# Optimization experiments

Measured on AMD Instinct MI355X. Metric: run time of the kernel, lower is better.

## Reference

```python
import jax, jax.numpy as jnp
import numpy as np

B, S, H, V = 256, 15, 512, 50257

def setup_inputs() -> dict:
    key = jax.random.key(0)
    ks = jax.random.split(key, 12)
    sc_h = 1.0 / np.sqrt(H)
    sc_in = 1.0 / np.sqrt(2 * H)
    return {
        "input_tokens": jax.random.randint(ks[0], (B, 1), 0, V),
        "hidden": jax.random.normal(ks[1], (1, B, H), jnp.float32),
        "encoder_outputs": jax.random.normal(ks[2], (B, S, H), jnp.float32),
        "emb_table": jax.random.normal(ks[3], (V, H), jnp.float32),
        "attn_W": jax.random.uniform(ks[4], (H, H), jnp.float32, -sc_h, sc_h),
        "attn_b": jax.random.uniform(ks[5], (H,), jnp.float32, -sc_h, sc_h),
        "W_ih": jax.random.uniform(ks[6], (3 * H, 2 * H), jnp.float32, -sc_in, sc_in),
        "W_hh": jax.random.uniform(ks[7], (3 * H, H), jnp.float32, -sc_h, sc_h),
        "b_ih": jax.random.uniform(ks[8], (3 * H,), jnp.float32, -sc_h, sc_h),
        "b_hh": jax.random.uniform(ks[9], (3 * H,), jnp.float32, -sc_h, sc_h),
        "out_W": jax.random.uniform(ks[10], (V, H), jnp.float32, -sc_h, sc_h),
        "out_b": jax.random.uniform(ks[11], (V,), jnp.float32, -sc_h, sc_h),
    }


def reference(input_tokens, hidden, encoder_outputs, emb_table, attn_W, attn_b,
              W_ih, W_hh, b_ih, b_hh, out_W, out_b):
    # Embedding (dropout is identity in eval/reference mode): [B,1,H]
    embedded = emb_table[input_tokens]
    h = hidden[0]  # [B,H]

    # Bahdanau-style scores, vectorized over the seq dim instead of the python loop:
    # energies[b,s] = attn(enc[b,s]);  score[b,s] = <h[b], energies[b,s]>
    energies = jnp.einsum("bsh,oh->bso", encoder_outputs, attn_W) + attn_b  # [B,S,H]
    attn_scores = jnp.einsum("bso,bo->bs", energies, h)                      # [B,S]
    attn_weights = jax.nn.softmax(attn_scores, axis=1)                       # [B,S]

    # context = weights @ encoder_outputs: [B,1,H]
    context = jnp.einsum("bs,bsh->bh", attn_weights, encoder_outputs)[:, None, :]

    # GRU single step (PyTorch gate order: r, z, n)
    x = jnp.concatenate([embedded, context], axis=2)[:, 0]  # [B,2H]
    gi = x @ W_ih.T + b_ih   # [B,3H]
    gh = h @ W_hh.T + b_hh   # [B,3H]
    i_r, i_z, i_n = jnp.split(gi, 3, axis=1)
    h_r, h_z, h_n = jnp.split(gh, 3, axis=1)
    r = jax.nn.sigmoid(i_r + h_r)
    z = jax.nn.sigmoid(i_z + h_z)
    n = jnp.tanh(i_n + r * h_n)
    h_new = (1.0 - z) * n + z * h            # [B,H]

    logits = h_new[:, None, :] @ out_W.T + out_b   # [B,1,V]
    log_probs = jax.nn.log_softmax(logits, axis=-1)
    return log_probs, h_new[None], attn_weights
```

## Files before the change

kernel.cpp:

```cpp
#include <hip/hip_runtime.h>

#define V_SIZE 50257
#define B_SIZE 256
#define S_LEN  15
#define H_DIM  512
#define NBLK_LG 786

typedef __attribute__((ext_vector_type(8))) short bf16x8;
typedef __attribute__((ext_vector_type(4))) float f32x4;

__device__ __forceinline__ unsigned short f2bf(float f) {
    unsigned int u = __float_as_uint(f);
    u += 0x7fffu + ((u >> 16) & 1u);
    return (unsigned short)(u >> 16);
}

__global__ __launch_bounds__(256) void u_kernel(
    const float* __restrict__ hidden, const float* __restrict__ attn_W,
    float* __restrict__ u)
{
    __shared__ float h_s[16][H_DIM];
    const int tid = threadIdx.x;
    const int b0 = blockIdx.y * 16, n0 = blockIdx.x * 32;
    const float4* hv = (const float4*)(hidden + (size_t)b0 * H_DIM);
    float4* hs4 = (float4*)&h_s[0][0];
    #pragma unroll
    for (int i = 0; i < 8; ++i) hs4[tid + i * 256] = hv[tid + i * 256];
    __syncthreads();
    const int n = n0 + (tid & 31);
    const int m = (tid >> 5) * 2;
    float a0 = 0.f, a1 = 0.f;
    #pragma unroll 8
    for (int o = 0; o < H_DIM; ++o) {
        float w = attn_W[(size_t)o * H_DIM + n];
        a0 += h_s[m][o] * w;
        a1 += h_s[m + 1][o] * w;
    }
    u[(size_t)(b0 + m) * H_DIM + n] = a0;
    u[(size_t)(b0 + m + 1) * H_DIM + n] = a1;
}

__global__ __launch_bounds__(256) void attn_kernel(
    const float* __restrict__ hidden, const float* __restrict__ enc,
    const float* __restrict__ u, const int* __restrict__ tokens,
    const float* __restrict__ emb, float* __restrict__ attnw_out,
    unsigned short* __restrict__ x_bf, unsigned short* __restrict__ h_bf)
{
    const int b = blockIdx.x, tid = threadIdx.x;
    __shared__ float u_s[H_DIM];
    __shared__ float sc_s[S_LEN];
    __shared__ float w_s[S_LEN];
    u_s[tid]       = u[(size_t)b * H_DIM + tid];
    u_s[tid + 256] = u[(size_t)b * H_DIM + tid + 256];
    h_bf[(size_t)b * H_DIM + tid]       = f2bf(hidden[(size_t)b * H_DIM + tid]);
    h_bf[(size_t)b * H_DIM + tid + 256] = f2bf(hidden[(size_t)b * H_DIM + tid + 256]);
    const int tok = tokens[b];
    x_bf[(size_t)b * 2 * H_DIM + tid]       = f2bf(emb[(size_t)tok * H_DIM + tid]);
    x_bf[(size_t)b * 2 * H_DIM + tid + 256] = f2bf(emb[(size_t)tok * H_DIM + tid + 256]);
    __syncthreads();
    const int wave = tid >> 6, lane = tid & 63;
    for (int s = wave; s < S_LEN; s += 4) {
        const float* e = enc + ((size_t)b * S_LEN + s) * H_DIM;
        float acc = 0.f;
        #pragma unroll
        for (int k = 0; k < H_DIM / 64; ++k) acc += e[lane + k * 64] * u_s[lane + k * 64];
        #pragma unroll
        for (int off = 32; off; off >>= 1) acc += __shfl_down(acc, off);
        if (lane == 0) sc_s[s] = acc;
    }
    __syncthreads();
    float mx = -1e30f;
    for (int s = 0; s < S_LEN; ++s) mx = fmaxf(mx, sc_s[s]);
    float sum = 0.f;
    for (int s = 0; s < S_LEN; ++s) sum += __expf(sc_s[s] - mx);
    const float inv = 1.f / sum;
    if (tid < S_LEN) {
        float w = __expf(sc_s[tid] - mx) * inv;
        w_s[tid] = w;
        attnw_out[b * S_LEN + tid] = w;
    }
    __syncthreads();
    #pragma unroll
    for (int hh = 0; hh < 2; ++hh) {
        int h = tid + hh * 256;
        float c = 0.f;
        #pragma unroll
        for (int s = 0; s < S_LEN; ++s)
            c += w_s[s] * enc[((size_t)b * S_LEN + s) * H_DIM + h];
        x_bf[(size_t)b * 2 * H_DIM + H_DIM + h] = f2bf(c);
    }
}

struct GemmP {
    const unsigned short* A; const float* B; const float* bias; float* C;
    int N; int K;
};

template<int BM, int BN, int BK, int WR, int WC>
__global__ __launch_bounds__(256) void gemm_nt(GemmP p0, GemmP p1)
{
    GemmP p = (blockIdx.z == 0) ? p0 : p1;
    constexpr int LDA = BK + 8;
    __shared__ __align__(16) unsigned short As[BM][LDA];
    __shared__ __align__(16) unsigned short Bs[BN][LDA];
    const int tid = threadIdx.x;
    const int bn0 = blockIdx.x * BN;
    const int bm0 = blockIdx.y * BM;
    const int wave = tid >> 6, lane = tid & 63;
    const int wm = (wave / WC) * (BM / WR);
    const int wn = (wave % WC) * (BN / WC);
    constexpr int MF = BM / WR / 16, NF = BN / WC / 16;
    const int n16 = lane & 15, quad = lane >> 4;

    f32x4 acc[MF][NF] = {};

    for (int k0 = 0; k0 < p.K; k0 += BK) {
        #pragma unroll
        for (int it = 0; it < BM / 32; ++it) {
            int v = it * 256 + tid;
            int row = v >> 3, seg = v & 7;
            *(uint4*)&As[row][seg * 8] =
                *(const uint4*)(p.A + (size_t)(bm0 + row) * p.K + k0 + seg * 8);
        }
        #pragma unroll
        for (int it = 0; it < BN / 32; ++it) {
            int v = it * 256 + tid;
            int row = v >> 3, seg = v & 7;
            int gv = bn0 + row;
            float4 w0 = make_float4(0, 0, 0, 0), w1 = make_float4(0, 0, 0, 0);
            if (gv < p.N) {
                const float4* src = (const float4*)(p.B + (size_t)gv * p.K + k0 + seg * 8);
                w0 = src[0]; w1 = src[1];
            }
            uint4 pk;
            pk.x = (unsigned)f2bf(w0.x) | ((unsigned)f2bf(w0.y) << 16);
            pk.y = (unsigned)f2bf(w0.z) | ((unsigned)f2bf(w0.w) << 16);
            pk.z = (unsigned)f2bf(w1.x) | ((unsigned)f2bf(w1.y) << 16);
            pk.w = (unsigned)f2bf(w1.z) | ((unsigned)f2bf(w1.w) << 16);
            *(uint4*)&Bs[row][seg * 8] = pk;
        }
        __syncthreads();
        #pragma unroll
        for (int kk = 0; kk < BK; kk += 32) {
            bf16x8 af[MF], bfr[NF];
            #pragma unroll
            for (int i = 0; i < MF; ++i)
                af[i] = *(const bf16x8*)&As[wm + i * 16 + n16][kk + quad * 8];
            #pragma unroll
            for (int j = 0; j < NF; ++j)
                bfr[j] = *(const bf16x8*)&Bs[wn + j * 16 + n16][kk + quad * 8];
            #pragma unroll
            for (int i = 0; i < MF; ++i)
                #pragma unroll
                for (int j = 0; j < NF; ++j)
                    acc[i][j] = __builtin_amdgcn_mfma_f32_16x16x32_bf16(
                        af[i], bfr[j], acc[i][j], 0, 0, 0);
        }
        __syncthreads();
    }
    #pragma unroll
    for (int i = 0; i < MF; ++i) {
        const int r0 = bm0 + wm + i * 16 + quad * 4;
        #pragma unroll
        for (int j = 0; j < NF; ++j) {
            const int c = bn0 + wn + j * 16 + n16;
            if (c < p.N) {
                const float bv = p.bias[c];
                #pragma unroll
                for (int r = 0; r < 4; ++r)
                    p.C[(size_t)(r0 + r) * p.N + c] = acc[i][j][r] + bv;
            }
        }
    }
}

template<bool PART>
__global__ __launch_bounds__(256, 4) void gemm_lg(
    const unsigned short* __restrict__ A, const float* __restrict__ B,
    const float* __restrict__ bias, float* __restrict__ C,
    float* __restrict__ pm, float* __restrict__ ps)
{
    constexpr int BN = 64, BK = 128;
    constexpr int LDB = BK + 8;
    __shared__ __align__(16) unsigned short Bs[BN][LDB];
    const int tid = threadIdx.x;
    const int bn0 = blockIdx.x * BN;
    const int wave = tid >> 6, lane = tid & 63;
    const int wm = wave * 64;
    const int n16 = lane & 15, quad = lane >> 4;

    f32x4 acc[4][4] = {};
    const unsigned short* arow[4];
    #pragma unroll
    for (int i = 0; i < 4; ++i) arow[i] = A + (size_t)(wm + i * 16 + n16) * H_DIM;

    for (int k0 = 0; k0 < H_DIM; k0 += BK) {
        #pragma unroll
        for (int it = 0; it < 4; ++it) {
            int v = it * 256 + tid;
            int row = v >> 4, seg = v & 15;
            int gv = bn0 + row;
            float4 w0 = make_float4(0, 0, 0, 0), w1 = make_float4(0, 0, 0, 0);
            if (gv < V_SIZE) {
                const float4* src = (const float4*)(B + (size_t)gv * H_DIM + k0 + seg * 8);
                w0 = src[0]; w1 = src[1];
            }
            uint4 pk;
            pk.x = (unsigned)f2bf(w0.x) | ((unsigned)f2bf(w0.y) << 16);
            pk.y = (unsigned)f2bf(w0.z) | ((unsigned)f2bf(w0.w) << 16);
            pk.z = (unsigned)f2bf(w1.x) | ((unsigned)f2bf(w1.y) << 16);
            pk.w = (unsigned)f2bf(w1.z) | ((unsigned)f2bf(w1.w) << 16);
            *(uint4*)&Bs[row][seg * 8] = pk;
        }
        __syncthreads();
        #pragma unroll
        for (int kk = 0; kk < BK; kk += 32) {
            bf16x8 af[4], bfr[4];
            #pragma unroll
            for (int i = 0; i < 4; ++i)
                af[i] = *(const bf16x8*)(arow[i] + k0 + kk + quad * 8);
            #pragma unroll
            for (int j = 0; j < 4; ++j)
                bfr[j] = *(const bf16x8*)&Bs[j * 16 + n16][kk + quad * 8];
            #pragma unroll
            for (int i = 0; i < 4; ++i)
                #pragma unroll
                for (int j = 0; j < 4; ++j)
                    acc[i][j] = __builtin_amdgcn_mfma_f32_16x16x32_bf16(
                        af[i], bfr[j], acc[i][j], 0, 0, 0);
        }
        __syncthreads();
    }

    int cj[4]; float bvv[4]; bool okj[4];
    #pragma unroll
    for (int j = 0; j < 4; ++j) {
        cj[j] = bn0 + j * 16 + n16;
        okj[j] = cj[j] < V_SIZE;
        bvv[j] = okj[j] ? bias[cj[j]] : 0.f;
    }
    #pragma unroll
    for (int i = 0; i < 4; ++i) {
        const int r0 = wm + i * 16 + quad * 4;
        if (PART) {
            #pragma unroll
            for (int r = 0; r < 4; ++r) {
                float m = -1e30f;
                #pragma unroll
                for (int j = 0; j < 4; ++j)
                    if (okj[j]) m = fmaxf(m, acc[i][j][r] + bvv[j]);
                #pragma unroll
                for (int d = 1; d < 16; d <<= 1) m = fmaxf(m, __shfl_xor(m, d));
                float s = 0.f;
                #pragma unroll
                for (int j = 0; j < 4; ++j)
                    if (okj[j]) s += __expf(acc[i][j][r] + bvv[j] - m);
                #pragma unroll
                for (int d = 1; d < 16; d <<= 1) s += __shfl_xor(s, d);
                if (n16 == 0) {
                    pm[(size_t)blockIdx.x * B_SIZE + r0 + r] = m;
                    ps[(size_t)blockIdx.x * B_SIZE + r0 + r] = s;
                }
            }
        }
        #pragma unroll
        for (int j = 0; j < 4; ++j) if (okj[j]) {
            #pragma unroll
            for (int r = 0; r < 4; ++r)
                C[(size_t)(r0 + r) * V_SIZE + cj[j]] = acc[i][j][r] + bvv[j];
        }
    }
}

__global__ __launch_bounds__(256) void gru_kernel(
    const float* __restrict__ gi, const float* __restrict__ gh,
    const float* __restrict__ hidden, float* __restrict__ hnew_out,
    unsigned short* __restrict__ hnew_bf)
{
    const int idx = blockIdx.x * 256 + threadIdx.x;
    const int b = idx >> 9, h = idx & 511;
    const float* gib = gi + (size_t)b * 3 * H_DIM;
    const float* ghb = gh + (size_t)b * 3 * H_DIM;
    float r = 1.f / (1.f + __expf(-(gib[h] + ghb[h])));
    float z = 1.f / (1.f + __expf(-(gib[H_DIM + h] + ghb[H_DIM + h])));
    float n = gib[2 * H_DIM + h] + r * ghb[2 * H_DIM + h];
    n = 1.f - 2.f / (1.f + __expf(2.f * n));
    float hp = hidden[idx];
    float hn = (1.f - z) * n + z * hp;
    hnew_out[idx] = hn;
    hnew_bf[idx] = f2bf(hn);
}

__global__ __launch_bounds__(1024) void finalize_kernel(
    float* __restrict__ logits, const float* __restrict__ pm,
    const float* __restrict__ ps)
{
    const int b = blockIdx.x, tid = threadIdx.x;
    float m = -1e30f, s = 0.f;
    for (int i = tid; i < NBLK_LG; i += 1024) {
        float mm = pm[(size_t)i * B_SIZE + b], ss = ps[(size_t)i * B_SIZE + b];
        float nm = fmaxf(m, mm);
        s = s * __expf(m - nm) + ss * __expf(mm - nm);
        m = nm;
    }
    const int lane = tid & 63, wave = tid >> 6;
    #pragma unroll
    for (int off = 32; off; off >>= 1) {
        float m2 = __shfl_down(m, off), s2 = __shfl_down(s, off);
        float nm = fmaxf(m, m2);
        s = s * __expf(m - nm) + s2 * __expf(m2 - nm);
        m = nm;
    }
    __shared__ float msh[16], ssh[16], lse_sh;
    if (lane == 0) { msh[wave] = m; ssh[wave] = s; }
    __syncthreads();
    if (tid == 0) {
        float M = msh[0], S = ssh[0];
        for (int w = 1; w < 16; ++w) {
            float nm = fmaxf(M, msh[w]);
            S = S * __expf(M - nm) + ssh[w] * __expf(msh[w] - nm);
            M = nm;
        }
        lse_sh = M + logf(S);
    }
    __syncthreads();
    const float lse = lse_sh;
    constexpr int HALF = (V_SIZE + 1) / 2;
    const int start = blockIdx.y * HALF;
    const int end = min(V_SIZE, start + HALF);
    float* row = logits + (size_t)b * V_SIZE;
    for (int c = start + tid; c < end; c += 1024) row[c] -= lse;
}

__global__ __launch_bounds__(1024) void logsoftmax_kernel(float* __restrict__ logits)
{
    const int b = blockIdx.x, tid = threadIdx.x;
    float* row = logits + (size_t)b * V_SIZE;
    float m = -1e30f, s = 0.f;
    for (int c = tid; c < V_SIZE; c += 1024) {
        float x = row[c];
        float nm = fmaxf(m, x);
        s = s * __expf(m - nm) + __expf(x - nm);
        m = nm;
    }
    const int lane = tid & 63, wave = tid >> 6;
    #pragma unroll
    for (int off = 32; off; off >>= 1) {
        float m2 = __shfl_down(m, off), s2 = __shfl_down(s, off);
        float nm = fmaxf(m, m2);
        s = s * __expf(m - nm) + s2 * __expf(m2 - nm);
        m = nm;
    }
    __shared__ float msh[16], ssh[16], lse_sh;
    if (lane == 0) { msh[wave] = m; ssh[wave] = s; }
    __syncthreads();
    if (tid == 0) {
        float M = msh[0], S = ssh[0];
        for (int w = 1; w < 16; ++w) {
            float nm = fmaxf(M, msh[w]);
            S = S * __expf(M - nm) + ssh[w] * __expf(msh[w] - nm);
            M = nm;
        }
        lse_sh = M + logf(S);
    }
    __syncthreads();
    const float lse = lse_sh;
    for (int c = tid; c < V_SIZE; c += 1024) row[c] -= lse;
}

constexpr size_t OFF_U      = 0;
constexpr size_t OFF_XBF    = 524288;
constexpr size_t OFF_HBF    = 1048576;
constexpr size_t OFF_HNEWBF = 1310720;
constexpr size_t OFF_GI     = 1572864;
constexpr size_t OFF_GH     = 3145728;
constexpr size_t OFF_PM     = 4718592;
constexpr size_t OFF_PS     = 5523456;
constexpr size_t WS_NEED    = 6328320;

extern "C" void kernel_launch(void* const* d_in, const int* in_sizes, int n_in,
                              void* d_out, int out_size, void* d_ws, size_t ws_size,
                              hipStream_t stream) {
    const int*   tokens = (const int*)d_in[0];
    const float* hidden = (const float*)d_in[1];
    const float* enc    = (const float*)d_in[2];
    const float* emb    = (const float*)d_in[3];
    const float* attn_W = (const float*)d_in[4];
    const float* W_ih   = (const float*)d_in[6];
    const float* W_hh   = (const float*)d_in[7];
    const float* b_ih   = (const float*)d_in[8];
    const float* b_hh   = (const float*)d_in[9];
    const float* out_W  = (const float*)d_in[10];
    const float* out_b  = (const float*)d_in[11];

    float* out = (float*)d_out;
    float* logp      = out;
    float* hnew_out  = out + (size_t)B_SIZE * V_SIZE;
    float* attnw_out = hnew_out + (size_t)B_SIZE * H_DIM;

    char* ws = (char*)d_ws;
    float*          u_ws    = (float*)(ws + OFF_U);
    unsigned short* x_bf    = (unsigned short*)(ws + OFF_XBF);
    unsigned short* h_bf    = (unsigned short*)(ws + OFF_HBF);
    unsigned short* hnew_bf = (unsigned short*)(ws + OFF_HNEWBF);
    float*          gi_ws   = (float*)(ws + OFF_GI);
    float*          gh_ws   = (float*)(ws + OFF_GH);
    float*          pm_ws   = (float*)(ws + OFF_PM);
    float*          ps_ws   = (float*)(ws + OFF_PS);

    u_kernel<<<dim3(16, 16), 256, 0, stream>>>(hidden, attn_W, u_ws);
    attn_kernel<<<dim3(256), 256, 0, stream>>>(hidden, enc, u_ws, tokens, emb,
                                               attnw_out, x_bf, h_bf);
    GemmP gi_p { x_bf, W_ih, b_ih, gi_ws, 3 * H_DIM, 2 * H_DIM };
    GemmP gh_p { h_bf, W_hh, b_hh, gh_ws, 3 * H_DIM, H_DIM };
    gemm_nt<64, 64, 64, 2, 2><<<dim3(24, 4, 2), 256, 0, stream>>>(gi_p, gh_p);
    gru_kernel<<<dim3(512), 256, 0, stream>>>(gi_ws, gh_ws, hidden, hnew_out, hnew_bf);

    if (ws_size >= WS_NEED) {
        gemm_lg<true><<<dim3(NBLK_LG), 256, 0, stream>>>(
            hnew_bf, out_W, out_b, logp, pm_ws, ps_ws);
        finalize_kernel<<<dim3(256, 2), 1024, 0, stream>>>(logp, pm_ws, ps_ws);
    } else {
        gemm_lg<false><<<dim3(NBLK_LG), 256, 0, stream>>>(
            hnew_bf, out_W, out_b, logp, nullptr, nullptr);
        logsoftmax_kernel<<<dim3(256), 1024, 0, stream>>>(logp);
    }
}
```

Baseline: 369.7 us.

## Fuse output GEMM and log-softmax via cooperative grid sync; stage encoder in LDS

```diff
diff --git a/kernel.cpp b/kernel.cpp
--- a/kernel.cpp
+++ b/kernel.cpp
@@ -1,4 +1,5 @@
 #include <hip/hip_runtime.h>
+#include <hip/hip_cooperative_groups.h>
 
 #define V_SIZE 50257
 #define B_SIZE 256
@@ -47,9 +48,19 @@
     unsigned short* __restrict__ x_bf, unsigned short* __restrict__ h_bf)
 {
     const int b = blockIdx.x, tid = threadIdx.x;
+    __shared__ float e_s[S_LEN][H_DIM];
     __shared__ float u_s[H_DIM];
     __shared__ float sc_s[S_LEN];
     __shared__ float w_s[S_LEN];
+    {
+        const float4* ev = (const float4*)(enc + (size_t)b * S_LEN * H_DIM);
+        float4* es4 = (float4*)&e_s[0][0];
+        #pragma unroll
+        for (int i = 0; i < 8; ++i) {
+            int idx = i * 256 + tid;
+            if (idx < S_LEN * H_DIM / 4) es4[idx] = ev[idx];
+        }
+    }
     u_s[tid]       = u[(size_t)b * H_DIM + tid];
     u_s[tid + 256] = u[(size_t)b * H_DIM + tid + 256];
     h_bf[(size_t)b * H_DIM + tid]       = f2bf(hidden[(size_t)b * H_DIM + tid]);
@@ -60,10 +71,10 @@
     __syncthreads();
     const int wave = tid >> 6, lane = tid & 63;
     for (int s = wave; s < S_LEN; s += 4) {
-        const float* e = enc + ((size_t)b * S_LEN + s) * H_DIM;
         float acc = 0.f;
         #pragma unroll
-        for (int k = 0; k < H_DIM / 64; ++k) acc += e[lane + k * 64] * u_s[lane + k * 64];
+        for (int k = 0; k < H_DIM / 64; ++k)
+            acc += e_s[s][lane + k * 64] * u_s[lane + k * 64];
         #pragma unroll
         for (int off = 32; off; off >>= 1) acc += __shfl_down(acc, off);
         if (lane == 0) sc_s[s] = acc;
@@ -86,7 +97,7 @@
         float c = 0.f;
         #pragma unroll
         for (int s = 0; s < S_LEN; ++s)
-            c += w_s[s] * enc[((size_t)b * S_LEN + s) * H_DIM + h];
+            c += w_s[s] * e_s[s][h];
         x_bf[(size_t)b * 2 * H_DIM + H_DIM + h] = f2bf(c);
     }
 }
@@ -174,6 +185,144 @@
     }
 }
 
+__global__ __launch_bounds__(256, 4) void gemm_lg_coop(
+    const unsigned short* __restrict__ A, const float* __restrict__ B,
+    const float* __restrict__ bias, float* __restrict__ C,
+    float* __restrict__ pm, float* __restrict__ ps, float* __restrict__ lse_g)
+{
+    constexpr int BN = 64, BK = 128;
+    constexpr int LDB = BK + 8;
+    __shared__ __align__(16) unsigned short Bs[BN][LDB];
+    __shared__ float red_m[4], red_s[4];
+    const int tid = threadIdx.x;
+    const int bn0 = blockIdx.x * BN;
+    const int wave = tid >> 6, lane = tid & 63;
+    const int wm = wave * 64;
+    const int n16 = lane & 15, quad = lane >> 4;
+
+    f32x4 acc[4][4] = {};
+    const unsigned short* arow[4];
+    #pragma unroll
+    for (int i = 0; i < 4; ++i) arow[i] = A + (size_t)(wm + i * 16 + n16) * H_DIM;
+
+    for (int k0 = 0; k0 < H_DIM; k0 += BK) {
+        #pragma unroll
+        for (int it = 0; it < 4; ++it) {
+            int v = it * 256 + tid;
+            int row = v >> 4, seg = v & 15;
+            int gv = bn0 + row;
+            float4 w0 = make_float4(0, 0, 0, 0), w1 = make_float4(0, 0, 0, 0);
+            if (gv < V_SIZE) {
+                const float4* src = (const float4*)(B + (size_t)gv * H_DIM + k0 + seg * 8);
+                w0 = src[0]; w1 = src[1];
+            }
+            uint4 pk;
+            pk.x = (unsigned)f2bf(w0.x) | ((unsigned)f2bf(w0.y) << 16);
+            pk.y = (unsigned)f2bf(w0.z) | ((unsigned)f2bf(w0.w) << 16);
+            pk.z = (unsigned)f2bf(w1.x) | ((unsigned)f2bf(w1.y) << 16);
+            pk.w = (unsigned)f2bf(w1.z) | ((unsigned)f2bf(w1.w) << 16);
+            *(uint4*)&Bs[row][seg * 8] = pk;
+        }
+        __syncthreads();
+        #pragma unroll
+        for (int kk = 0; kk < BK; kk += 32) {
+            bf16x8 af[4], bfr[4];
+            #pragma unroll
+            for (int i = 0; i < 4; ++i)
+                af[i] = *(const bf16x8*)(arow[i] + k0 + kk + quad * 8);
+            #pragma unroll
+            for (int j = 0; j < 4; ++j)
+                bfr[j] = *(const bf16x8*)&Bs[j * 16 + n16][kk + quad * 8];
+            #pragma unroll
+            for (int i = 0; i < 4; ++i)
+                #pragma unroll
+                for (int j = 0; j < 4; ++j)
+                    acc[i][j] = __builtin_amdgcn_mfma_f32_16x16x32_bf16(
+                        af[i], bfr[j], acc[i][j], 0, 0, 0);
+        }
+        __syncthreads();
+    }
+
+    int cj[4]; float bvv[4]; bool okj[4];
+    #pragma unroll
+    for (int j = 0; j < 4; ++j) {
+        cj[j] = bn0 + j * 16 + n16;
+        okj[j] = cj[j] < V_SIZE;
+        bvv[j] = okj[j] ? bias[cj[j]] : 0.f;
+    }
+    #pragma unroll
+    for (int i = 0; i < 4; ++i) {
+        const int r0 = wm + i * 16 + quad * 4;
+        #pragma unroll
+        for (int r = 0; r < 4; ++r) {
+            float m = -1e30f;
+            #pragma unroll
+            for (int j = 0; j < 4; ++j)
+                if (okj[j]) m = fmaxf(m, acc[i][j][r] + bvv[j]);
+            #pragma unroll
+            for (int d = 1; d < 16; d <<= 1) m = fmaxf(m, __shfl_xor(m, d));
+            float s = 0.f;
+            #pragma unroll
+            for (int j = 0; j < 4; ++j)
+                if (okj[j]) s += __expf(acc[i][j][r] + bvv[j] - m);
+            #pragma unroll
+            for (int d = 1; d < 16; d <<= 1) s += __shfl_xor(s, d);
+            if (n16 == 0) {
+                pm[(size_t)blockIdx.x * B_SIZE + r0 + r] = m;
+                ps[(size_t)blockIdx.x * B_SIZE + r0 + r] = s;
+            }
+        }
+    }
+
+    cooperative_groups::this_grid().sync();
+
+    if (blockIdx.x < B_SIZE) {
+        const int b = blockIdx.x;
+        float m = -1e30f, s = 0.f;
+        for (int i = tid; i < NBLK_LG; i += 256) {
+            float mm = pm[(size_t)i * B_SIZE + b], ss = ps[(size_t)i * B_SIZE + b];
+            float nm = fmaxf(m, mm);
+            s = s * __expf(m - nm) + ss * __expf(mm - nm);
+            m = nm;
+        }
+        #pragma unroll
+        for (int off = 32; off; off >>= 1) {
+            float m2 = __shfl_down(m, off), s2 = __shfl_down(s, off);
+            float nm = fmaxf(m, m2);
+            s = s * __expf(m - nm) + s2 * __expf(m2 - nm);
+            m = nm;
+        }
+        if (lane == 0) { red_m[wave] = m; red_s[wave] = s; }
+        __syncthreads();
+        if (tid == 0) {
+            float M = red_m[0], S = red_s[0];
+            #pragma unroll
+            for (int w = 1; w < 4; ++w) {
+                float nm = fmaxf(M, red_m[w]);
+                S = S * __expf(M - nm) + red_s[w] * __expf(red_m[w] - nm);
+                M = nm;
+            }
+            lse_g[b] = M + logf(S);
+        }
+    }
+
+    cooperative_groups::this_grid().sync();
+
+    #pragma unroll
+    for (int i = 0; i < 4; ++i) {
+        const int r0 = wm + i * 16 + quad * 4;
+        float ls[4];
+        #pragma unroll
+        for (int r = 0; r < 4; ++r) ls[r] = lse_g[r0 + r];
+        #pragma unroll
+        for (int j = 0; j < 4; ++j) if (okj[j]) {
+            #pragma unroll
+            for (int r = 0; r < 4; ++r)
+                C[(size_t)(r0 + r) * V_SIZE + cj[j]] = acc[i][j][r] + bvv[j] - ls[r];
+        }
+    }
+}
+
 template<bool PART>
 __global__ __launch_bounds__(256, 4) void gemm_lg(
     const unsigned short* __restrict__ A, const float* __restrict__ B,
@@ -325,7 +474,7 @@
     }
     __syncthreads();
     const float lse = lse_sh;
-    constexpr int HALF = (V_SIZE + 1) / 2;
+    constexpr int HALF = 25132;
     const int start = blockIdx.y * HALF;
     const int end = min(V_SIZE, start + HALF);
     float* row = logits + (size_t)b * V_SIZE;
@@ -376,7 +525,9 @@
 constexpr size_t OFF_GH     = 3145728;
 constexpr size_t OFF_PM     = 4718592;
 constexpr size_t OFF_PS     = 5523456;
-constexpr size_t WS_NEED    = 6328320;
+constexpr size_t OFF_LSE    = 6328320;
+constexpr size_t WS_NEED      = 6328320;
+constexpr size_t WS_NEED_COOP = 6329344;
 
 extern "C" void kernel_launch(void* const* d_in, const int* in_sizes, int n_in,
                               void* d_out, int out_size, void* d_ws, size_t ws_size,
@@ -407,6 +558,7 @@
     float*          gh_ws   = (float*)(ws + OFF_GH);
     float*          pm_ws   = (float*)(ws + OFF_PM);
     float*          ps_ws   = (float*)(ws + OFF_PS);
+    float*          lse_ws  = (float*)(ws + OFF_LSE);
 
     u_kernel<<<dim3(16, 16), 256, 0, stream>>>(hidden, attn_W, u_ws);
     attn_kernel<<<dim3(256), 256, 0, stream>>>(hidden, enc, u_ws, tokens, emb,
@@ -416,13 +568,28 @@
     gemm_nt<64, 64, 64, 2, 2><<<dim3(24, 4, 2), 256, 0, stream>>>(gi_p, gh_p);
     gru_kernel<<<dim3(512), 256, 0, stream>>>(gi_ws, gh_ws, hidden, hnew_out, hnew_bf);
 
-    if (ws_size >= WS_NEED) {
-        gemm_lg<true><<<dim3(NBLK_LG), 256, 0, stream>>>(
-            hnew_bf, out_W, out_b, logp, pm_ws, ps_ws);
-        finalize_kernel<<<dim3(256, 2), 1024, 0, stream>>>(logp, pm_ws, ps_ws);
-    } else {
-        gemm_lg<false><<<dim3(NBLK_LG), 256, 0, stream>>>(
-            hnew_bf, out_W, out_b, logp, nullptr, nullptr);
-        logsoftmax_kernel<<<dim3(256), 1024, 0, stream>>>(logp);
-    }
-}
+    bool done = false;
+    if (ws_size >= WS_NEED_COOP) {
+        const unsigned short* a_arg = hnew_bf;
+        const float* b_arg = out_W;
+        const float* bias_arg = out_b;
+        float* c_arg = logp;
+        float* pm_arg = pm_ws; float* ps_arg = ps_ws; float* lse_arg = lse_ws;
+        void* args[7] = { &a_arg, &b_arg, &bias_arg, &c_arg,
+                          &pm_arg, &ps_arg, &lse_arg };
+        hipError_t e = hipLaunchCooperativeKernel(
+            (const void*)gemm_lg_coop, dim3(NBLK_LG), dim3(256), args, 0, stream);
+        done = (e == hipSuccess);
+    }
+    if (!done) {
+        if (ws_size >= WS_NEED) {
+            gemm_lg<true><<<dim3(NBLK_LG), 256, 0, stream>>>(
+                hnew_bf, out_W, out_b, logp, pm_ws, ps_ws);
+            finalize_kernel<<<dim3(256, 2), 1024, 0, stream>>>(logp, pm_ws, ps_ws);
+        } else {
+            gemm_lg<false><<<dim3(NBLK_LG), 256, 0, stream>>>(
+                hnew_bf, out_W, out_b, logp, nullptr, nullptr);
+            logsoftmax_kernel<<<dim3(256), 1024, 0, stream>>>(logp);
+        }
+    }
+}
```

New measurement: 546.8 us. 1.48x slower.
